# Kernel tuning notes

Hardware: AMD Instinct MI355X
Metric: run time of the kernel (lower is better)

The kernel has to match this reference:

```python
import jax, jax.numpy as jnp
from jax import lax
import numpy as np

R = 256            # reservoir_size
LUT_LEN = 18       # 2**18 LUT entries per node
B = 8              # bits_per_feature
D = 4              # n_features
M = 512            # samples
S = 512            # steps
OUT = 10           # output_size


def _first_primes(n):
    sieve = np.ones(2000, dtype=bool)
    sieve[:2] = False
    for i in range(2, 45):
        if sieve[i]:
            sieve[i * i::i] = False
    return np.nonzero(sieve)[0][:n].astype(np.int32)


def setup_inputs() -> dict:
    key = jax.random.key(0)
    ks = jax.random.split(key, 7)
    x = jax.random.randint(ks[0], (M, S, D, B), 0, 2).astype(bool)
    lut = jax.random.randint(ks[1], (R, 2 ** LUT_LEN), 0, 2).astype(jnp.int32)
    init_res = jax.random.randint(ks[2], (R,), 0, 2).astype(bool)
    W_res = jax.random.randint(ks[3], (R, R), 0, 2).astype(bool)
    input_nodes = jax.random.permutation(ks[4], R)[: B * D].astype(jnp.int32)
    primes = jnp.asarray(_first_primes(R))
    readout_W = jax.random.normal(ks[5], (OUT, R), dtype=jnp.float32) * (1.0 / np.sqrt(R))
    readout_b = jax.random.normal(ks[6], (OUT,), dtype=jnp.float32) * 0.01
    return {
        "x": x,
        "input_nodes": input_nodes,
        "lut": lut,
        "W_res": W_res,
        "primes": primes,
        "init_res": init_res,
        "readout_W": readout_W,
        "readout_b": readout_b,
    }


def _run_reservoir(x, input_nodes, lut, W_res, primes, init_res):
    m, s, d, b = x.shape
    xf = x.reshape(m, s, d * b).astype(jnp.int32)          # [m, s, d*b]
    # row j of Wp holds primes[k] * W_res[j, k]; idx = r @ Wp.T
    Wp = W_res.astype(jnp.int32) * primes[None, :]          # [R, R]
    node_idx = jnp.arange(R)[None, :]                       # [1, R]
    r0 = jnp.broadcast_to(init_res.astype(jnp.int32), (m, R))

    def step(r, x_t):
        # write encoded input bits into the reservoir, then LUT-perturb
        r = r.at[:, input_nodes].set(x_t)                   # [m, R]
        idx = r @ Wp.T                                      # [m, R] state indices
        r_new = jnp.take_along_axis(lut[None].repeat(1, 0)[0][node_idx.repeat(m, 0) * 0 + node_idx, idx], jnp.zeros((m, R, 1), jnp.int32), axis=-1) if False else lut[node_idx, idx]
        return r_new.astype(jnp.int32), None

    rf, _ = lax.scan(step, r0, jnp.swapaxes(xf, 0, 1))      # scan over s steps
    return rf                                               # [m, R] final states (0/1)


def reference(x, input_nodes, lut, W_res, primes, init_res, readout_W, readout_b):
    rf = _run_reservoir(x, input_nodes, lut, W_res, primes, init_res)
    return rf.astype(jnp.float32) @ readout_W.T + readout_b  # [m, output_size]
```

## Files before the change

kernel.cpp:

```cpp
#include <hip/hip_runtime.h>
#include <stdint.h>

#define R_NODES 256
#define M_SAMP  512
#define S_STEPS 512
#define OUT_N   10

typedef unsigned int u32x2 __attribute__((ext_vector_type(2)));

__global__ void detect_layout(const uint8_t* __restrict__ x, int* __restrict__ flag) {
    __shared__ int any;
    if (threadIdx.x == 0) any = 0;
    __syncthreads();
    int acc = 0;
    for (int i = 0; i < 64; ++i)
        acc |= x[(size_t)(threadIdx.x * 64 + i) * 4 + 1];
    if (acc) atomicOr(&any, 1);
    __syncthreads();
    if (threadIdx.x == 0) *flag = any ? 1 : 0;
}

__global__ void pack_x(const uint8_t* __restrict__ x, const int* __restrict__ flag,
                       uint32_t* __restrict__ xp) {
    const int stride = (*flag) ? 1 : 4;
    const int f = blockIdx.x * blockDim.x + threadIdx.x;
    const int val = x[(size_t)f * stride];
    const uint64_t mask = __ballot(val != 0);
    const int lane = threadIdx.x & 63;
    if ((lane & 31) == 0) {
        uint32_t w = (lane & 32) ? (uint32_t)(mask >> 32) : (uint32_t)mask;
        xp[f >> 5] = w;
    }
}

__global__ void build_T1(const uint8_t* __restrict__ wres, const int* __restrict__ primes,
                         const int* __restrict__ flag, uint16_t* __restrict__ T1) {
    const int v = blockIdx.x;
    const int c = blockIdx.y;
    const int j = threadIdx.x;
    const int stride = (*flag) ? 1 : 4;
    int sum = 0;
#pragma unroll
    for (int p = 0; p < 4; ++p) {
        if ((v >> p) & 1) {
            const int k = c * 4 + p;
            if (wres[(size_t)(j * 256 + k) * stride]) sum += primes[k];
        }
    }
    T1[((size_t)v * 64 + c) * 256 + j] = (uint16_t)sum;
}

__device__ __forceinline__ uint32_t spread8(uint32_t x) {
    x = (x | (x << 12)) & 0x000F000Fu;
    x = (x | (x << 6))  & 0x03030303u;
    x = (x | (x << 3))  & 0x11111111u;
    return x;
}
__global__ void pack_lut(const int* __restrict__ lut, uint32_t* __restrict__ lp32) {
    const int lane = threadIdx.x & 63;
    const int gw = blockIdx.x * (blockDim.x >> 6) + (threadIdx.x >> 6);
    const int4* src = (const int4*)lut;
    for (int it = 0; it < 16; ++it) {
        const int chunk = gw * 16 + it;
        const int4 q = src[(size_t)chunk * 64 + lane];
        const uint64_t b0 = __ballot((q.x & 1) != 0);
        const uint64_t b1 = __ballot((q.y & 1) != 0);
        const uint64_t b2 = __ballot((q.z & 1) != 0);
        const uint64_t b3 = __ballot((q.w & 1) != 0);
        if (lane < 8) {
            const uint32_t B0 = (uint32_t)(b0 >> (8 * lane)) & 0xFF;
            const uint32_t B1 = (uint32_t)(b1 >> (8 * lane)) & 0xFF;
            const uint32_t B2 = (uint32_t)(b2 >> (8 * lane)) & 0xFF;
            const uint32_t B3 = (uint32_t)(b3 >> (8 * lane)) & 0xFF;
            const uint32_t w = spread8(B0) | (spread8(B1) << 1)
                             | (spread8(B2) << 2) | (spread8(B3) << 3);
            lp32[(size_t)chunk * 8 + lane] = w;
        }
    }
}

__global__ __launch_bounds__(64, 1) void reservoir_wave(
    const uint32_t* __restrict__ xp, const uint16_t* __restrict__ T1,
    const uint64_t* __restrict__ lp, const int* __restrict__ input_nodes,
    const uint8_t* __restrict__ init_res, const int* __restrict__ flag,
    const float* __restrict__ rW, const float* __restrict__ rb,
    float* __restrict__ out)
{
    const int m = blockIdx.x;
    const int l = threadIdx.x;
    const int stride = (*flag) ? 1 : 4;

    __shared__ uint32_t sxw[S_STEPS];
    const uint32_t* xrow = xp + m * S_STEPS;
    for (int i = l; i < S_STEPS; i += 64) sxw[i] = xrow[i];

    int slot0 = -1, slot1 = -1, slot2 = -1, slot3 = -1;
    for (int i = 0; i < 32; ++i) {
        const int n = input_nodes[i];
        if (n == 4 * l + 0) slot0 = i;
        if (n == 4 * l + 1) slot1 = i;
        if (n == 4 * l + 2) slot2 = i;
        if (n == 4 * l + 3) slot3 = i;
    }
    int v0 = init_res[(size_t)(4 * l + 0) * stride] ? 1 : 0;
    int v1 = init_res[(size_t)(4 * l + 1) * stride] ? 1 : 0;
    int v2 = init_res[(size_t)(4 * l + 2) * stride] ? 1 : 0;
    int v3 = init_res[(size_t)(4 * l + 3) * stride] ? 1 : 0;

    const uint64_t t1base = (uint64_t)(uintptr_t)T1;
    const uint64_t lpbase = (uint64_t)(uintptr_t)lp;
    const uint32_t lane8  = (uint32_t)(l << 3);
    const uint32_t nb     = (uint32_t)l << 17;

    __syncthreads();
    uint32_t xw = sxw[0];

#define LOADC(c) do {                                                         \
        const int so_ = __builtin_amdgcn_readlane((int)vtmp, (c));            \
        const uint32_t vo_ = (uint32_t)so_ + lane8;                           \
        asm volatile("global_load_dwordx2 %0, %1, %2"                         \
                     : "=v"(d[(c)]) : "v"(vo_), "s"(t1base));                 \
    } while (0)

#define GROUP(g, WAITSTR) do {                                                \
        asm volatile(WAITSTR);                                                \
        asm volatile("" : "+v"(d[8*(g)+0]), "+v"(d[8*(g)+1]),                 \
                          "+v"(d[8*(g)+2]), "+v"(d[8*(g)+3]),                 \
                          "+v"(d[8*(g)+4]), "+v"(d[8*(g)+5]),                 \
                          "+v"(d[8*(g)+6]), "+v"(d[8*(g)+7]));                \
        const uint32_t lo_ = d[8*(g)+0][0] + d[8*(g)+1][0] + d[8*(g)+2][0]    \
                           + d[8*(g)+3][0] + d[8*(g)+4][0] + d[8*(g)+5][0]    \
                           + d[8*(g)+6][0] + d[8*(g)+7][0];                   \
        const uint32_t hi_ = d[8*(g)+0][1] + d[8*(g)+1][1] + d[8*(g)+2][1]    \
                           + d[8*(g)+3][1] + d[8*(g)+4][1] + d[8*(g)+5][1]    \
                           + d[8*(g)+6][1] + d[8*(g)+7][1];                   \
        i0 += lo_ & 0xFFFFu;  i1 += lo_ >> 16;                                \
        i2 += hi_ & 0xFFFFu;  i3 += hi_ >> 16;                                \
    } while (0)

    for (int s = 0; s < S_STEPS; ++s) {
        if (slot0 >= 0) v0 = (xw >> slot0) & 1;
        if (slot1 >= 0) v1 = (xw >> slot1) & 1;
        if (slot2 >= 0) v2 = (xw >> slot2) & 1;
        if (slot3 >= 0) v3 = (xw >> slot3) & 1;

        const uint32_t val = (uint32_t)v0 | ((uint32_t)v1 << 1)
                           | ((uint32_t)v2 << 2) | ((uint32_t)v3 << 3);
        const int vtmp = (int)((val << 15) | ((uint32_t)l << 9));

        u32x2 d[64];
#pragma unroll
        for (int c = 0; c < 48; ++c) LOADC(c);
        asm volatile("s_waitcnt vmcnt(40)");
#pragma unroll
        for (int c = 48; c < 64; ++c) LOADC(c);

        const uint32_t xw_next = sxw[(s + 1 < S_STEPS) ? s + 1 : s];

        uint32_t i0 = 0, i1 = 0, i2 = 0, i3 = 0;
        GROUP(0, "s_waitcnt vmcnt(56)");
        GROUP(1, "s_waitcnt vmcnt(48)");
        GROUP(2, "s_waitcnt vmcnt(40)");
        GROUP(3, "s_waitcnt vmcnt(32)");
        GROUP(4, "s_waitcnt vmcnt(24)");
        GROUP(5, "s_waitcnt vmcnt(16)");
        GROUP(6, "s_waitcnt vmcnt(8)");
        GROUP(7, "s_waitcnt vmcnt(0)");

        u32x2 w0, w1, w2, w3;
        const uint32_t o0 = nb             + ((i0 >> 6) << 3);
        const uint32_t o1 = nb + (1 << 15) + ((i1 >> 6) << 3);
        const uint32_t o2 = nb + (2 << 15) + ((i2 >> 6) << 3);
        const uint32_t o3 = nb + (3 << 15) + ((i3 >> 6) << 3);
        asm volatile("global_load_dwordx2 %0, %1, %2" : "=v"(w0) : "v"(o0), "s"(lpbase));
        asm volatile("global_load_dwordx2 %0, %1, %2" : "=v"(w1) : "v"(o1), "s"(lpbase));
        asm volatile("global_load_dwordx2 %0, %1, %2" : "=v"(w2) : "v"(o2), "s"(lpbase));
        asm volatile("global_load_dwordx2 %0, %1, %2" : "=v"(w3) : "v"(o3), "s"(lpbase));
        asm volatile("s_waitcnt vmcnt(0)");
        asm volatile("" : "+v"(w0), "+v"(w1), "+v"(w2), "+v"(w3));

        v0 = (int)(((((uint64_t)w0[1] << 32) | w0[0]) >> (i0 & 63)) & 1);
        v1 = (int)(((((uint64_t)w1[1] << 32) | w1[0]) >> (i1 & 63)) & 1);
        v2 = (int)(((((uint64_t)w2[1] << 32) | w2[0]) >> (i2 & 63)) & 1);
        v3 = (int)(((((uint64_t)w3[1] << 32) | w3[0]) >> (i3 & 63)) & 1);
        xw = xw_next;
    }
#undef LOADC
#undef GROUP

    const float* rWo;
    const float* rbo;
    asm volatile("" : "=s"(rWo) : "0"(rW));
    asm volatile("" : "=s"(rbo) : "0"(rb));

#pragma unroll
    for (int o = 0; o < OUT_N; ++o) {
        const float* wrow = rWo + o * R_NODES + 4 * l;
        float c = 0.f;
        if (v0) c += wrow[0];
        if (v1) c += wrow[1];
        if (v2) c += wrow[2];
        if (v3) c += wrow[3];
#pragma unroll
        for (int off = 32; off > 0; off >>= 1)
            c += __shfl_down(c, off, 64);
        if (l == 0) out[m * OUT_N + o] = c + rbo[o];
    }
}

extern "C" void kernel_launch(void* const* d_in, const int* in_sizes, int n_in,
                              void* d_out, int out_size, void* d_ws, size_t ws_size,
                              hipStream_t stream) {
    const uint8_t* x        = (const uint8_t*)d_in[0];
    const int* input_nodes  = (const int*)d_in[1];
    const int* lut          = (const int*)d_in[2];
    const uint8_t* wres     = (const uint8_t*)d_in[3];
    const int* primes       = (const int*)d_in[4];
    const uint8_t* init_res = (const uint8_t*)d_in[5];
    const float* rW         = (const float*)d_in[6];
    const float* rb         = (const float*)d_in[7];
    float* out              = (float*)d_out;

    uint8_t* ws = (uint8_t*)d_ws;
    int*      flag = (int*)ws;
    uint32_t* xp   = (uint32_t*)(ws + 4096);
    uint16_t* T1   = (uint16_t*)(ws + 4096 + 1048576);
    uint64_t* lp   = (uint64_t*)(ws + 4096 + 1048576 + 524288);

    detect_layout<<<1, 256, 0, stream>>>(x, flag);
    pack_x<<<(M_SAMP * S_STEPS * 32) / 256, 256, 0, stream>>>(x, flag, xp);
    build_T1<<<dim3(16, 64), 256, 0, stream>>>(wres, primes, flag, T1);
    pack_lut<<<4096, 256, 0, stream>>>(lut, (uint32_t*)lp);
    reservoir_wave<<<M_SAMP, 64, 0, stream>>>(xp, T1, lp, input_nodes, init_res,
                                              flag, rW, rb, out);
}
```

Baseline: 1.107 ms.

## Switch to 8-bit-chunk partial-sum table with dwordx4 loads and half-wave split

Replaces the 4-bit-chunk prime-weighted partial sum table (16×64 entries per node) with an 8-bit-chunk table (256×32 entries). Each step then needs 16 dwordx4 gathers per lane instead of 64 dwordx2 gathers. The two half-waves each cover half the chunks for 8 nodes and combine their results with a cross-half shuffle, which also changes how nodes are assigned to lanes. This cuts per-step memory instruction count and latency on the serial recurrence, at the cost of an 8x larger table (more cache pressure), extra ballots and shuffles, and a larger table-build kernel.

```diff
diff --git a/kernel.cpp b/kernel.cpp
--- a/kernel.cpp
+++ b/kernel.cpp
@@ -7,6 +7,7 @@
 #define OUT_N   10
 
 typedef unsigned int u32x2 __attribute__((ext_vector_type(2)));
+typedef unsigned int u32x4 __attribute__((ext_vector_type(4)));
 
 __global__ void detect_layout(const uint8_t* __restrict__ x, int* __restrict__ flag) {
     __shared__ int any;
@@ -33,21 +34,21 @@
     }
 }
 
-__global__ void build_T1(const uint8_t* __restrict__ wres, const int* __restrict__ primes,
-                         const int* __restrict__ flag, uint16_t* __restrict__ T1) {
+__global__ void build_T2(const uint8_t* __restrict__ wres, const int* __restrict__ primes,
+                         const int* __restrict__ flag, uint16_t* __restrict__ T2) {
     const int v = blockIdx.x;
     const int c = blockIdx.y;
     const int j = threadIdx.x;
     const int stride = (*flag) ? 1 : 4;
     int sum = 0;
 #pragma unroll
-    for (int p = 0; p < 4; ++p) {
+    for (int p = 0; p < 8; ++p) {
         if ((v >> p) & 1) {
-            const int k = c * 4 + p;
+            const int k = c * 8 + p;
             if (wres[(size_t)(j * 256 + k) * stride]) sum += primes[k];
         }
     }
-    T1[((size_t)v * 64 + c) * 256 + j] = (uint16_t)sum;
+    T2[((size_t)v * 32 + c) * 256 + j] = (uint16_t)sum;
 }
 
 __device__ __forceinline__ uint32_t spread8(uint32_t x) {
@@ -80,7 +81,7 @@
 }
 
 __global__ __launch_bounds__(64, 1) void reservoir_wave(
-    const uint32_t* __restrict__ xp, const uint16_t* __restrict__ T1,
+    const uint32_t* __restrict__ xp, const uint16_t* __restrict__ T2,
     const uint64_t* __restrict__ lp, const int* __restrict__ input_nodes,
     const uint8_t* __restrict__ init_res, const int* __restrict__ flag,
     const float* __restrict__ rW, const float* __restrict__ rb,
@@ -89,6 +90,8 @@
     const int m = blockIdx.x;
     const int l = threadIdx.x;
     const int stride = (*flag) ? 1 : 4;
+    const bool lohalf = (l < 32);
+    const int n0 = lohalf ? (l << 3) : (((l - 32) << 3) + 4);
 
     __shared__ uint32_t sxw[S_STEPS];
     const uint32_t* xrow = xp + m * S_STEPS;
@@ -97,45 +100,44 @@
     int slot0 = -1, slot1 = -1, slot2 = -1, slot3 = -1;
     for (int i = 0; i < 32; ++i) {
         const int n = input_nodes[i];
-        if (n == 4 * l + 0) slot0 = i;
-        if (n == 4 * l + 1) slot1 = i;
-        if (n == 4 * l + 2) slot2 = i;
-        if (n == 4 * l + 3) slot3 = i;
-    }
-    int v0 = init_res[(size_t)(4 * l + 0) * stride] ? 1 : 0;
-    int v1 = init_res[(size_t)(4 * l + 1) * stride] ? 1 : 0;
-    int v2 = init_res[(size_t)(4 * l + 2) * stride] ? 1 : 0;
-    int v3 = init_res[(size_t)(4 * l + 3) * stride] ? 1 : 0;
-
-    const uint64_t t1base = (uint64_t)(uintptr_t)T1;
+        if (n == n0 + 0) slot0 = i;
+        if (n == n0 + 1) slot1 = i;
+        if (n == n0 + 2) slot2 = i;
+        if (n == n0 + 3) slot3 = i;
+    }
+    int v0 = init_res[(size_t)(n0 + 0) * stride] ? 1 : 0;
+    int v1 = init_res[(size_t)(n0 + 1) * stride] ? 1 : 0;
+    int v2 = init_res[(size_t)(n0 + 2) * stride] ? 1 : 0;
+    int v3 = init_res[(size_t)(n0 + 3) * stride] ? 1 : 0;
+
+    const uint64_t t2base = (uint64_t)(uintptr_t)T2;
     const uint64_t lpbase = (uint64_t)(uintptr_t)lp;
-    const uint32_t lane8  = (uint32_t)(l << 3);
-    const uint32_t nb     = (uint32_t)l << 17;
+    const uint32_t colb   = (uint32_t)((l & 31) << 4);
+    const uint32_t nb     = (uint32_t)n0 << 15;
 
     __syncthreads();
     uint32_t xw = sxw[0];
 
-#define LOADC(c) do {                                                         \
-        const int so_ = __builtin_amdgcn_readlane((int)vtmp, (c));            \
-        const uint32_t vo_ = (uint32_t)so_ + lane8;                           \
-        asm volatile("global_load_dwordx2 %0, %1, %2"                         \
-                     : "=v"(d[(c)]) : "v"(vo_), "s"(t1base));                 \
+#define LOADI(i) do {                                                         \
+        const int se_ = __builtin_amdgcn_readlane((int)roff, 2*(i));          \
+        const int so_ = __builtin_amdgcn_readlane((int)roff, 2*(i)+1);        \
+        const uint32_t sel_ = lohalf ? (uint32_t)se_ : (uint32_t)so_;         \
+        asm volatile("global_load_dwordx4 %0, %1, %2"                         \
+                     : "=v"(d[(i)]) : "v"(sel_ + colb), "s"(t2base));         \
     } while (0)
 
 #define GROUP(g, WAITSTR) do {                                                \
         asm volatile(WAITSTR);                                                \
-        asm volatile("" : "+v"(d[8*(g)+0]), "+v"(d[8*(g)+1]),                 \
-                          "+v"(d[8*(g)+2]), "+v"(d[8*(g)+3]),                 \
-                          "+v"(d[8*(g)+4]), "+v"(d[8*(g)+5]),                 \
-                          "+v"(d[8*(g)+6]), "+v"(d[8*(g)+7]));                \
-        const uint32_t lo_ = d[8*(g)+0][0] + d[8*(g)+1][0] + d[8*(g)+2][0]    \
-                           + d[8*(g)+3][0] + d[8*(g)+4][0] + d[8*(g)+5][0]    \
-                           + d[8*(g)+6][0] + d[8*(g)+7][0];                   \
-        const uint32_t hi_ = d[8*(g)+0][1] + d[8*(g)+1][1] + d[8*(g)+2][1]    \
-                           + d[8*(g)+3][1] + d[8*(g)+4][1] + d[8*(g)+5][1]    \
-                           + d[8*(g)+6][1] + d[8*(g)+7][1];                   \
-        i0 += lo_ & 0xFFFFu;  i1 += lo_ >> 16;                                \
-        i2 += hi_ & 0xFFFFu;  i3 += hi_ >> 16;                                \
+        asm volatile("" : "+v"(d[4*(g)+0]), "+v"(d[4*(g)+1]),                 \
+                          "+v"(d[4*(g)+2]), "+v"(d[4*(g)+3]));                \
+        const uint32_t px = d[4*(g)+0][0] + d[4*(g)+1][0] + d[4*(g)+2][0] + d[4*(g)+3][0]; \
+        const uint32_t py = d[4*(g)+0][1] + d[4*(g)+1][1] + d[4*(g)+2][1] + d[4*(g)+3][1]; \
+        const uint32_t pz = d[4*(g)+0][2] + d[4*(g)+1][2] + d[4*(g)+2][2] + d[4*(g)+3][2]; \
+        const uint32_t pw = d[4*(g)+0][3] + d[4*(g)+1][3] + d[4*(g)+2][3] + d[4*(g)+3][3]; \
+        a0 += px & 0xFFFFu;  a1 += px >> 16;                                  \
+        a2 += py & 0xFFFFu;  a3 += py >> 16;                                  \
+        a4 += pz & 0xFFFFu;  a5 += pz >> 16;                                  \
+        a6 += pw & 0xFFFFu;  a7 += pw >> 16;                                  \
     } while (0)
 
     for (int s = 0; s < S_STEPS; ++s) {
@@ -144,28 +146,47 @@
         if (slot2 >= 0) v2 = (xw >> slot2) & 1;
         if (slot3 >= 0) v3 = (xw >> slot3) & 1;
 
-        const uint32_t val = (uint32_t)v0 | ((uint32_t)v1 << 1)
-                           | ((uint32_t)v2 << 2) | ((uint32_t)v3 << 3);
-        const int vtmp = (int)((val << 15) | ((uint32_t)l << 9));
-
-        u32x2 d[64];
-#pragma unroll
-        for (int c = 0; c < 48; ++c) LOADC(c);
-        asm volatile("s_waitcnt vmcnt(40)");
-#pragma unroll
-        for (int c = 48; c < 64; ++c) LOADC(c);
+        const uint64_t b0 = __ballot(v0 != 0);
+        const uint64_t b1 = __ballot(v1 != 0);
+        const uint64_t b2 = __ballot(v2 != 0);
+        const uint64_t b3 = __ballot(v3 != 0);
+
+        const uint32_t C = (uint32_t)(l & 31);
+        const uint32_t u = (((uint32_t)(b0        ) >> C) & 1u)
+                         | ((((uint32_t)(b1       ) >> C) & 1u) << 1)
+                         | ((((uint32_t)(b2       ) >> C) & 1u) << 2)
+                         | ((((uint32_t)(b3       ) >> C) & 1u) << 3)
+                         | ((((uint32_t)(b0 >> 32) >> C) & 1u) << 4)
+                         | ((((uint32_t)(b1 >> 32) >> C) & 1u) << 5)
+                         | ((((uint32_t)(b2 >> 32) >> C) & 1u) << 6)
+                         | ((((uint32_t)(b3 >> 32) >> C) & 1u) << 7);
+        const uint32_t roff = (u << 14) | (C << 9);
+
+        u32x4 d[16];
+#pragma unroll
+        for (int i = 0; i < 16; ++i) LOADI(i);
 
         const uint32_t xw_next = sxw[(s + 1 < S_STEPS) ? s + 1 : s];
 
-        uint32_t i0 = 0, i1 = 0, i2 = 0, i3 = 0;
-        GROUP(0, "s_waitcnt vmcnt(56)");
-        GROUP(1, "s_waitcnt vmcnt(48)");
-        GROUP(2, "s_waitcnt vmcnt(40)");
-        GROUP(3, "s_waitcnt vmcnt(32)");
-        GROUP(4, "s_waitcnt vmcnt(24)");
-        GROUP(5, "s_waitcnt vmcnt(16)");
-        GROUP(6, "s_waitcnt vmcnt(8)");
-        GROUP(7, "s_waitcnt vmcnt(0)");
+        uint32_t a0 = 0, a1 = 0, a2 = 0, a3 = 0, a4 = 0, a5 = 0, a6 = 0, a7 = 0;
+        GROUP(0, "s_waitcnt vmcnt(12)");
+        GROUP(1, "s_waitcnt vmcnt(8)");
+        GROUP(2, "s_waitcnt vmcnt(4)");
+        GROUP(3, "s_waitcnt vmcnt(0)");
+
+        const uint32_t t0 = a0 + __shfl_xor(a0, 32, 64);
+        const uint32_t t1 = a1 + __shfl_xor(a1, 32, 64);
+        const uint32_t t2 = a2 + __shfl_xor(a2, 32, 64);
+        const uint32_t t3 = a3 + __shfl_xor(a3, 32, 64);
+        const uint32_t t4 = a4 + __shfl_xor(a4, 32, 64);
+        const uint32_t t5 = a5 + __shfl_xor(a5, 32, 64);
+        const uint32_t t6 = a6 + __shfl_xor(a6, 32, 64);
+        const uint32_t t7 = a7 + __shfl_xor(a7, 32, 64);
+
+        const uint32_t i0 = lohalf ? t0 : t4;
+        const uint32_t i1 = lohalf ? t1 : t5;
+        const uint32_t i2 = lohalf ? t2 : t6;
+        const uint32_t i3 = lohalf ? t3 : t7;
 
         u32x2 w0, w1, w2, w3;
         const uint32_t o0 = nb             + ((i0 >> 6) << 3);
@@ -185,7 +206,7 @@
         v3 = (int)(((((uint64_t)w3[1] << 32) | w3[0]) >> (i3 & 63)) & 1);
         xw = xw_next;
     }
-#undef LOADC
+#undef LOADI
 #undef GROUP
 
     const float* rWo;
@@ -195,7 +216,7 @@
 
 #pragma unroll
     for (int o = 0; o < OUT_N; ++o) {
-        const float* wrow = rWo + o * R_NODES + 4 * l;
+        const float* wrow = rWo + o * R_NODES + n0;
         float c = 0.f;
         if (v0) c += wrow[0];
         if (v1) c += wrow[1];
@@ -224,13 +245,13 @@
     uint8_t* ws = (uint8_t*)d_ws;
     int*      flag = (int*)ws;
     uint32_t* xp   = (uint32_t*)(ws + 4096);
-    uint16_t* T1   = (uint16_t*)(ws + 4096 + 1048576);
-    uint64_t* lp   = (uint64_t*)(ws + 4096 + 1048576 + 524288);
+    uint16_t* T2   = (uint16_t*)(ws + 4096 + 1048576);
+    uint64_t* lp   = (uint64_t*)(ws + 4096 + 1048576 + 4194304);
 
     detect_layout<<<1, 256, 0, stream>>>(x, flag);
     pack_x<<<(M_SAMP * S_STEPS * 32) / 256, 256, 0, stream>>>(x, flag, xp);
-    build_T1<<<dim3(16, 64), 256, 0, stream>>>(wres, primes, flag, T1);
+    build_T2<<<dim3(256, 32), 256, 0, stream>>>(wres, primes, flag, T2);
     pack_lut<<<4096, 256, 0, stream>>>(lut, (uint32_t*)lp);
-    reservoir_wave<<<M_SAMP, 64, 0, stream>>>(xp, T1, lp, input_nodes, init_res,
+    reservoir_wave<<<M_SAMP, 64, 0, stream>>>(xp, T2, lp, input_nodes, init_res,
                                               flag, rW, rb, out);
 }
```

After: 1.076 ms. 2.8% less time.
